# Kernel tuning notes

Hardware: AMD Instinct MI355X
Metric: run time of the kernel (lower is better)

Reference implementation:

```python
import jax, jax.numpy as jnp
import numpy as np

M, K, N, G = 4096, 4096, 4096, 128


def setup_inputs() -> dict:
    key = jax.random.key(0)
    k1, k2, k3 = jax.random.split(key, 3)
    a = jax.random.normal(k1, (M, K), dtype=jnp.float16)
    # 4-bit unsigned quantized weights, values in [0, 16)
    w_q = jax.random.randint(k2, (K, N), 0, 16, dtype=jnp.int32)
    # group-wise scales: one per (k-group, n); small magnitude keeps fp16 output in range
    scale = jax.random.uniform(k3, (K // G, N), dtype=jnp.float16, minval=0.001, maxval=0.02)
    return {"a": a, "w_q": w_q, "scale": scale, "group_size": G}


def reference(a, w_q, scale, group_size):
    # Dequantize: w[k, n] = w_q[k, n] * scale[k // group_size, n]
    scale_full = jnp.repeat(scale, group_size, axis=0)  # [K, N]
    w = w_q.astype(a.dtype) * scale_full                # fp16 dequantized weight
    out = jnp.matmul(a, w, preferred_element_type=jnp.float32)
    return out.astype(jnp.float16)
```

## Files before the change

### kernel.cpp

```cpp
#include <hip/hip_runtime.h>
#include <hip/hip_fp16.h>

#define MDIM 4096
#define NDIM 4096
#define KDIM 4096
#define NT 256

typedef _Float16 f16x8 __attribute__((ext_vector_type(8)));
typedef float f32x4 __attribute__((ext_vector_type(4)));
typedef unsigned int u32;
typedef unsigned short u16;

__device__ inline __half2 as_half2(u32 u) { return __builtin_bit_cast(__half2, u); }
__device__ inline u32 as_u32(__half2 h) { return __builtin_bit_cast(u32, h); }
__device__ inline u32 pkrtz(float a, float b) {
  return __builtin_bit_cast(u32, __builtin_amdgcn_cvt_pkrtz(a, b));
}

__device__ inline void load16_to_lds(const void* g, void* l) {
  __builtin_amdgcn_global_load_lds(
      (__attribute__((address_space(1))) const u32*)g,
      (__attribute__((address_space(3))) u32*)l,
      16, 0, 0);
}

template <int VM>
__device__ __forceinline__ void wait_vmcnt() {
  if constexpr (VM == 8)
    asm volatile("s_waitcnt vmcnt(8)" ::: "memory");
  else if constexpr (VM == 4)
    asm volatile("s_waitcnt vmcnt(4)" ::: "memory");
  else
    asm volatile("s_waitcnt vmcnt(0)" ::: "memory");
}

__global__ __launch_bounds__(NT) void prep_a(const float* __restrict__ A,
                                             _Float16* __restrict__ A16) {
  const size_t base = ((size_t)blockIdx.x * NT + threadIdx.x) * 8;
  const float4 f0 = *(const float4*)(A + base);
  const float4 f1 = *(const float4*)(A + base + 4);
  u32 pk[4];
  pk[0] = pkrtz(f0.x, f0.y);
  pk[1] = pkrtz(f0.z, f0.w);
  pk[2] = pkrtz(f1.x, f1.y);
  pk[3] = pkrtz(f1.z, f1.w);
  *(uint4*)(A16 + base) = *(const uint4*)pk;
}

#define TSTR 68
__global__ __launch_bounds__(NT) void prep_w(const int* __restrict__ Wq,
                                             const float* __restrict__ Sc,
                                             _Float16* __restrict__ Wt) {
  __shared__ __align__(16) u16 Ls[64 * TSTR];
  const int tid = threadIdx.x;
  const int n0 = (blockIdx.x & 63) * 64;
  const int k0 = (blockIdx.x >> 6) * 64;
  const int g = k0 >> 7;

#pragma unroll
  for (int r = 0; r < 4; ++r) {
    const int c = r * 256 + tid;
    const int krow = c >> 4;
    const int col4 = (c & 15) * 4;
    const int4 v = *(const int4*)(Wq + (size_t)(k0 + krow) * NDIM + n0 + col4);
    const float4 s = *(const float4*)(Sc + (size_t)g * NDIM + n0 + col4);
    __half2 s01 = __floats2half2_rn(s.x, s.y);
    __half2 s23 = __floats2half2_rn(s.z, s.w);
    const __half2 kneg = __half2half2(__float2half(-1024.0f));
    __half2 nb01 = __hmul2(s01, kneg), nb23 = __hmul2(s23, kneg);
    u32 u01 = (u32)v.x | ((u32)v.y << 16) | 0x64006400u;
    u32 u23 = (u32)v.z | ((u32)v.w << 16) | 0x64006400u;
    u32 pk[2];
    pk[0] = as_u32(__hfma2(as_half2(u01), s01, nb01));
    pk[1] = as_u32(__hfma2(as_half2(u23), s23, nb23));
    *(uint2*)&Ls[(size_t)krow * TSTR + col4] = *(const uint2*)pk;
  }
  __syncthreads();

#pragma unroll
  for (int r = 0; r < 2; ++r) {
    const int idx = r * 256 + tid;
    const int n = idx >> 3;
    const int kc = (idx & 7) * 8;
    u16 tmp[8];
#pragma unroll
    for (int j = 0; j < 8; ++j) tmp[j] = Ls[(size_t)(kc + j) * TSTR + n];
    *(uint4*)(Wt + (size_t)(n0 + n) * KDIM + k0 + kc) = *(const uint4*)tmp;
  }
}

__global__ __launch_bounds__(512, 2) void gemm_f16(const _Float16* __restrict__ A16,
                                                   const _Float16* __restrict__ Wt,
                                                   float* __restrict__ C) {
  __shared__ __align__(16) _Float16 As[4 * 256 * 32];
  __shared__ __align__(16) _Float16 Bs[4 * 256 * 32];

  const int tid = threadIdx.x;
  const int bx = blockIdx.x & 15;
  const int by = blockIdx.x >> 4;
  const int m_base = by * 256;
  const int n_base = bx * 256;

  const int wave = tid >> 6;
  const int lane = tid & 63;
  const int l15 = lane & 15;
  const int quad = lane >> 4;
  const int mq = wave >> 2;
  const int nq = wave & 3;
  const int gq = (l15 >> 1) & 3;
  const int pchunk = quad ^ gq;

  f32x4 acc[8][4];
#pragma unroll
  for (int i = 0; i < 8; ++i)
#pragma unroll
    for (int j = 0; j < 4; ++j) acc[i][j] = (f32x4)0.0f;

  auto stage = [&](int p) {
    const int T = p >> 1;
    const int h = p & 1;
    const int s = p & 3;
    const size_t kof = (size_t)T * 64 + (size_t)h * 32;
#pragma unroll
    for (int L = 0; L < 2; ++L) {
      const int cc = L * 512 + tid;
      const int row = cc >> 2;
      const int lch = (cc & 3) ^ ((row >> 1) & 3);
      load16_to_lds(A16 + (size_t)(m_base + row) * KDIM + kof + lch * 8,
                    (char*)As + (size_t)s * 16384 + (size_t)cc * 16);
    }
#pragma unroll
    for (int L = 0; L < 2; ++L) {
      const int cc = L * 512 + tid;
      const int row = cc >> 2;
      const int lch = (cc & 3) ^ ((row >> 1) & 3);
      load16_to_lds(Wt + (size_t)(n_base + row) * KDIM + kof + lch * 8,
                    (char*)Bs + (size_t)s * 16384 + (size_t)cc * 16);
    }
  };

  auto phase_body = [&](int p, bool dostage) {
    __builtin_amdgcn_s_barrier();
    asm volatile("" ::: "memory");
    const int s = p & 3;
    const _Float16* Ab = (const _Float16*)((const char*)As + (size_t)s * 16384);
    const _Float16* Bb = (const _Float16*)((const char*)Bs + (size_t)s * 16384);
    f16x8 af[8], bf[4];
#pragma unroll
    for (int i = 0; i < 8; ++i) {
      const int row = mq * 128 + i * 16 + l15;
      af[i] = *(const f16x8*)(Ab + (size_t)row * 32 + pchunk * 8);
    }
#pragma unroll
    for (int j = 0; j < 4; ++j) {
      const int row = nq * 64 + j * 16 + l15;
      bf[j] = *(const f16x8*)(Bb + (size_t)row * 32 + pchunk * 8);
    }
    if (dostage) stage(p + 3);
    asm volatile("s_waitcnt lgkmcnt(0)" ::: "memory");
    __builtin_amdgcn_sched_barrier(0);
    __builtin_amdgcn_s_setprio(1);
#pragma unroll
    for (int i = 0; i < 8; ++i)
#pragma unroll
      for (int j = 0; j < 4; ++j)
        acc[i][j] = __builtin_amdgcn_mfma_f32_16x16x32_f16(af[i], bf[j],
                                                           acc[i][j], 0, 0, 0);
    __builtin_amdgcn_s_setprio(0);
  };

  stage(0);
  stage(1);
  stage(2);

  for (int p = 0; p < 125; ++p) {
    wait_vmcnt<8>();
    phase_body(p, true);
  }
  wait_vmcnt<8>();
  phase_body(125, false);
  wait_vmcnt<4>();
  phase_body(126, false);
  wait_vmcnt<0>();
  phase_body(127, false);

#pragma unroll
  for (int i = 0; i < 8; ++i) {
#pragma unroll
    for (int j = 0; j < 4; ++j) {
      const int col = n_base + nq * 64 + j * 16 + l15;
#pragma unroll
      for (int r = 0; r < 4; ++r) {
        const int row = m_base + mq * 128 + i * 16 + quad * 4 + r;
        C[(size_t)row * NDIM + col] = __half2float(__float2half(acc[i][j][r]));
      }
    }
  }
}

#define STR 72
__global__ __launch_bounds__(NT) void qgemm_fused(
    const float* __restrict__ A, const int* __restrict__ Wq,
    const float* __restrict__ Sc, float* __restrict__ C) {
  __shared__ __align__(16) _Float16 As[128 * STR];
  __shared__ __align__(16) _Float16 Bs[128 * STR];
  const int tid = threadIdx.x;
  const int bx = blockIdx.x & 31, by = blockIdx.x >> 5;
  const int m_base = by * 128, n_base = bx * 128;
  const int wave = tid >> 6, lane = tid & 63;
  const int l15 = lane & 15, quad = lane >> 4;
  const int wm = (wave & 1) * 64, wn = (wave >> 1) * 64;
  const int bn_local = tid & 127, bk_half = (tid >> 7) * 8;
  const int gn = n_base + bn_local;
  f32x4 acc[4][4];
#pragma unroll
  for (int i = 0; i < 4; ++i)
#pragma unroll
    for (int j = 0; j < 4; ++j) acc[i][j] = (f32x4)0.0f;
  for (int kt = 0; kt < KDIM / 64; ++kt) {
    const int k0 = kt * 64;
    __syncthreads();
#pragma unroll
    for (int i = 0; i < 8; ++i) {
      const int c = i * 256 + tid;
      const int row = c >> 4, col4 = (c & 15) * 4;
      const float4 f = *(const float4*)(A + (size_t)(m_base + row) * KDIM + k0 + col4);
      u32 pk[2];
      pk[0] = pkrtz(f.x, f.y);
      pk[1] = pkrtz(f.z, f.w);
      *(uint2*)&As[(size_t)row * STR + col4] = *(const uint2*)pk;
    }
    {
      const __half hs = __float2half(Sc[(size_t)(k0 >> 7) * NDIM + gn]);
      const __half2 s2 = __half2half2(hs);
      const __half2 nb2 = __half2half2(__hmul(hs, __float2half(-1024.0f)));
#pragma unroll
      for (int it = 0; it < 4; ++it) {
        const int k = bk_half + it * 16;
        u32 v[8];
#pragma unroll
        for (int j = 0; j < 8; ++j)
          v[j] = (u32)Wq[(size_t)(k0 + k + j) * NDIM + gn];
        u32 pk[4];
#pragma unroll
        for (int p = 0; p < 4; ++p) {
          u32 u = v[2 * p] | (v[2 * p + 1] << 16) | 0x64006400u;
          pk[p] = as_u32(__hfma2(as_half2(u), s2, nb2));
        }
        *(uint4*)&Bs[(size_t)bn_local * STR + k] = *(const uint4*)pk;
      }
    }
    __syncthreads();
#pragma unroll
    for (int ks = 0; ks < 64; ks += 32) {
      f16x8 af[4], bf[4];
#pragma unroll
      for (int i = 0; i < 4; ++i)
        af[i] = *(const f16x8*)&As[(size_t)(wm + i * 16 + l15) * STR + ks + quad * 8];
#pragma unroll
      for (int j = 0; j < 4; ++j)
        bf[j] = *(const f16x8*)&Bs[(size_t)(wn + j * 16 + l15) * STR + ks + quad * 8];
#pragma unroll
      for (int i = 0; i < 4; ++i)
#pragma unroll
        for (int j = 0; j < 4; ++j)
          acc[i][j] = __builtin_amdgcn_mfma_f32_16x16x32_f16(af[i], bf[j],
                                                             acc[i][j], 0, 0, 0);
    }
  }
#pragma unroll
  for (int i = 0; i < 4; ++i)
#pragma unroll
    for (int j = 0; j < 4; ++j) {
      const int col = n_base + wn + j * 16 + l15;
#pragma unroll
      for (int r = 0; r < 4; ++r) {
        const int row = m_base + wm + i * 16 + quad * 4 + r;
        C[(size_t)row * NDIM + col] = __half2float(__float2half(acc[i][j][r]));
      }
    }
}

extern "C" void kernel_launch(void* const* d_in, const int* in_sizes, int n_in,
                              void* d_out, int out_size, void* d_ws, size_t ws_size,
                              hipStream_t stream) {
  const float* a = (const float*)d_in[0];
  const int* wq = (const int*)d_in[1];
  const float* sc = (const float*)d_in[2];
  float* out = (float*)d_out;

  const size_t a16_bytes = (size_t)MDIM * KDIM * 2;
  const size_t wt_bytes = (size_t)NDIM * KDIM * 2;

  if (ws_size >= a16_bytes + wt_bytes) {
    _Float16* a16 = (_Float16*)d_ws;
    _Float16* wt = (_Float16*)((char*)d_ws + a16_bytes);
    prep_a<<<(MDIM * KDIM) / (NT * 8), NT, 0, stream>>>(a, a16);
    prep_w<<<(KDIM / 64) * (NDIM / 64), NT, 0, stream>>>(wq, sc, wt);
    gemm_f16<<<(MDIM / 256) * (NDIM / 256), 512, 0, stream>>>(a16, wt, out);
  } else {
    qgemm_fused<<<(MDIM / 128) * (NDIM / 128), NT, 0, stream>>>(a, wq, sc, out);
  }
}
```

Before: 291.0 us.

## Fuse int4 weight dequantization into GEMM B-tile staging, drop prep_w kernel

```diff
diff --git a/kernel.cpp b/kernel.cpp
--- a/kernel.cpp
+++ b/kernel.cpp
@@ -26,10 +26,15 @@
 
 template <int VM>
 __device__ __forceinline__ void wait_vmcnt() {
-  if constexpr (VM == 8)
-    asm volatile("s_waitcnt vmcnt(8)" ::: "memory");
+  static_assert(VM == 0 || VM == 2 || VM == 4 || VM == 17 || VM == 21, "");
+  if constexpr (VM == 21)
+    asm volatile("s_waitcnt vmcnt(21)" ::: "memory");
+  else if constexpr (VM == 17)
+    asm volatile("s_waitcnt vmcnt(17)" ::: "memory");
   else if constexpr (VM == 4)
     asm volatile("s_waitcnt vmcnt(4)" ::: "memory");
+  else if constexpr (VM == 2)
+    asm volatile("s_waitcnt vmcnt(2)" ::: "memory");
   else
     asm volatile("s_waitcnt vmcnt(0)" ::: "memory");
 }
@@ -47,50 +52,9 @@
   *(uint4*)(A16 + base) = *(const uint4*)pk;
 }
 
-#define TSTR 68
-__global__ __launch_bounds__(NT) void prep_w(const int* __restrict__ Wq,
-                                             const float* __restrict__ Sc,
-                                             _Float16* __restrict__ Wt) {
-  __shared__ __align__(16) u16 Ls[64 * TSTR];
-  const int tid = threadIdx.x;
-  const int n0 = (blockIdx.x & 63) * 64;
-  const int k0 = (blockIdx.x >> 6) * 64;
-  const int g = k0 >> 7;
-
-#pragma unroll
-  for (int r = 0; r < 4; ++r) {
-    const int c = r * 256 + tid;
-    const int krow = c >> 4;
-    const int col4 = (c & 15) * 4;
-    const int4 v = *(const int4*)(Wq + (size_t)(k0 + krow) * NDIM + n0 + col4);
-    const float4 s = *(const float4*)(Sc + (size_t)g * NDIM + n0 + col4);
-    __half2 s01 = __floats2half2_rn(s.x, s.y);
-    __half2 s23 = __floats2half2_rn(s.z, s.w);
-    const __half2 kneg = __half2half2(__float2half(-1024.0f));
-    __half2 nb01 = __hmul2(s01, kneg), nb23 = __hmul2(s23, kneg);
-    u32 u01 = (u32)v.x | ((u32)v.y << 16) | 0x64006400u;
-    u32 u23 = (u32)v.z | ((u32)v.w << 16) | 0x64006400u;
-    u32 pk[2];
-    pk[0] = as_u32(__hfma2(as_half2(u01), s01, nb01));
-    pk[1] = as_u32(__hfma2(as_half2(u23), s23, nb23));
-    *(uint2*)&Ls[(size_t)krow * TSTR + col4] = *(const uint2*)pk;
-  }
-  __syncthreads();
-
-#pragma unroll
-  for (int r = 0; r < 2; ++r) {
-    const int idx = r * 256 + tid;
-    const int n = idx >> 3;
-    const int kc = (idx & 7) * 8;
-    u16 tmp[8];
-#pragma unroll
-    for (int j = 0; j < 8; ++j) tmp[j] = Ls[(size_t)(kc + j) * TSTR + n];
-    *(uint4*)(Wt + (size_t)(n0 + n) * KDIM + k0 + kc) = *(const uint4*)tmp;
-  }
-}
-
 __global__ __launch_bounds__(512, 2) void gemm_f16(const _Float16* __restrict__ A16,
-                                                   const _Float16* __restrict__ Wt,
+                                                   const int* __restrict__ Wq,
+                                                   const float* __restrict__ Sc,
                                                    float* __restrict__ C) {
   __shared__ __align__(16) _Float16 As[4 * 256 * 32];
   __shared__ __align__(16) _Float16 Bs[4 * 256 * 32];
@@ -110,17 +74,47 @@
   const int gq = (l15 >> 1) & 3;
   const int pchunk = quad ^ gq;
 
+  const int bn = tid & 255;
+  const int kh = (tid >> 8) * 16;
+  const int swzn = (bn >> 1) & 3;
+  const int c0p = (kh >> 3) ^ swzn;
+  const int* const wq_col = Wq + n_base + bn;
+  const float* const sc_col = Sc + n_base + bn;
+
   f32x4 acc[8][4];
 #pragma unroll
   for (int i = 0; i < 8; ++i)
 #pragma unroll
     for (int j = 0; j < 4; ++j) acc[i][j] = (f32x4)0.0f;
 
-  auto stage = [&](int p) {
-    const int T = p >> 1;
-    const int h = p & 1;
-    const int s = p & 3;
-    const size_t kof = (size_t)T * 64 + (size_t)h * 32;
+  int vb0[16], vb1[16];
+  float sc0, sc1;
+
+  auto issueB = [&](int q, int(&vb)[16], float& sc) {
+    const int* src = wq_col + (size_t)(q * 32 + kh) * NDIM;
+#pragma unroll
+    for (int l = 0; l < 16; ++l) vb[l] = src[(size_t)l * NDIM];
+    sc = sc_col[(size_t)(q >> 2) * NDIM];
+  };
+
+  auto writeB = [&](int q, int(&vb)[16], float sc) {
+    const __half hs = __float2half(sc);
+    const __half2 s2 = __half2half2(hs);
+    const __half2 nb = __half2half2(__hmul(hs, __float2half(-1024.0f)));
+    u32 pk[8];
+#pragma unroll
+    for (int l = 0; l < 8; ++l) {
+      const u32 u = (u32)vb[2 * l] | ((u32)vb[2 * l + 1] << 16) | 0x64006400u;
+      pk[l] = as_u32(__hfma2(as_half2(u), s2, nb));
+    }
+    char* slotb = (char*)Bs + (size_t)(q & 3) * 16384 + (size_t)bn * 64;
+    *(uint4*)(slotb + c0p * 16) = *(const uint4*)&pk[0];
+    *(uint4*)(slotb + (c0p ^ 1) * 16) = *(const uint4*)&pk[4];
+  };
+
+  auto issueA = [&](int q) {
+    const size_t kof = (size_t)q * 32;
+    const int s = q & 3;
 #pragma unroll
     for (int L = 0; L < 2; ++L) {
       const int cc = L * 512 + tid;
@@ -129,17 +123,9 @@
       load16_to_lds(A16 + (size_t)(m_base + row) * KDIM + kof + lch * 8,
                     (char*)As + (size_t)s * 16384 + (size_t)cc * 16);
     }
-#pragma unroll
-    for (int L = 0; L < 2; ++L) {
-      const int cc = L * 512 + tid;
-      const int row = cc >> 2;
-      const int lch = (cc & 3) ^ ((row >> 1) & 3);
-      load16_to_lds(Wt + (size_t)(n_base + row) * KDIM + kof + lch * 8,
-                    (char*)Bs + (size_t)s * 16384 + (size_t)cc * 16);
-    }
   };
 
-  auto phase_body = [&](int p, bool dostage) {
+  auto phase = [&](int p, int(&vb)[16], float& sc, bool dw, bool dib, bool dia) {
     __builtin_amdgcn_s_barrier();
     asm volatile("" ::: "memory");
     const int s = p & 3;
@@ -156,7 +142,9 @@
       const int row = nq * 64 + j * 16 + l15;
       bf[j] = *(const f16x8*)(Bb + (size_t)row * 32 + pchunk * 8);
     }
-    if (dostage) stage(p + 3);
+    if (dw) writeB(p + 2, vb, sc);
+    if (dib) issueB(p + 4, vb, sc);
+    if (dia) issueA(p + 3);
     asm volatile("s_waitcnt lgkmcnt(0)" ::: "memory");
     __builtin_amdgcn_sched_barrier(0);
     __builtin_amdgcn_s_setprio(1);
@@ -169,20 +157,36 @@
     __builtin_amdgcn_s_setprio(0);
   };
 
-  stage(0);
-  stage(1);
-  stage(2);
-
-  for (int p = 0; p < 125; ++p) {
-    wait_vmcnt<8>();
-    phase_body(p, true);
+  issueB(0, vb0, sc0);
+  issueB(1, vb1, sc1);
+  wait_vmcnt<17>();
+  writeB(0, vb0, sc0);
+  issueB(2, vb0, sc0);
+  wait_vmcnt<17>();
+  writeB(1, vb1, sc1);
+  issueB(3, vb1, sc1);
+  issueA(0);
+  issueA(1);
+  issueA(2);
+
+  wait_vmcnt<4>();
+  phase(0, vb0, sc0, true, true, true);
+  for (int p = 1; p < 123; p += 2) {
+    wait_vmcnt<21>();
+    phase(p, vb1, sc1, true, true, true);
+    wait_vmcnt<21>();
+    phase(p + 1, vb0, sc0, true, true, true);
   }
-  wait_vmcnt<8>();
-  phase_body(125, false);
+  wait_vmcnt<21>();
+  phase(123, vb1, sc1, true, true, true);
+  wait_vmcnt<21>();
+  phase(124, vb0, sc0, true, false, true);
   wait_vmcnt<4>();
-  phase_body(126, false);
+  phase(125, vb1, sc1, true, false, false);
+  wait_vmcnt<2>();
+  phase(126, vb0, sc0, false, false, false);
   wait_vmcnt<0>();
-  phase_body(127, false);
+  phase(127, vb1, sc1, false, false, false);
 
 #pragma unroll
   for (int i = 0; i < 8; ++i) {
@@ -290,14 +294,11 @@
   float* out = (float*)d_out;
 
   const size_t a16_bytes = (size_t)MDIM * KDIM * 2;
-  const size_t wt_bytes = (size_t)NDIM * KDIM * 2;
-
-  if (ws_size >= a16_bytes + wt_bytes) {
+
+  if (ws_size >= a16_bytes) {
     _Float16* a16 = (_Float16*)d_ws;
-    _Float16* wt = (_Float16*)((char*)d_ws + a16_bytes);
     prep_a<<<(MDIM * KDIM) / (NT * 8), NT, 0, stream>>>(a, a16);
-    prep_w<<<(KDIM / 64) * (NDIM / 64), NT, 0, stream>>>(wq, sc, wt);
-    gemm_f16<<<(MDIM / 256) * (NDIM / 256), 512, 0, stream>>>(a16, wt, out);
+    gemm_f16<<<(MDIM / 256) * (NDIM / 256), 512, 0, stream>>>(a16, wq, sc, out);
   } else {
     qgemm_fused<<<(MDIM / 128) * (NDIM / 128), NT, 0, stream>>>(a, wq, sc, out);
   }
```

After: 329.2 us. 13.1% more time.
